# Kernel optimization log

Hardware: AMD Instinct MI355X
Metric: run time of the kernel (lower is better)

The kernel has to match this reference:

```python
import jax, jax.numpy as jnp
import numpy as np

DIM = 2048
N_HEADS = 16
N_KV_HEADS = 4
HEAD_DIM = DIM // N_HEADS  # 128
ROPE_BASE = 10000.0
QK_GAIN_INIT = 1.0
RMS_EPS = 1.1920928955078125e-07  # torch F.rms_norm default eps = finfo(fp32).eps


def _rms_norm(x):
    # normalize over last dim, no learned gain
    var = jnp.mean(jnp.square(x), axis=-1, keepdims=True)
    return x * jax.lax.rsqrt(var + RMS_EPS)


def _rope_cos_sin(seq_len, dtype):
    half = HEAD_DIM // 2
    inv_freq = 1.0 / (ROPE_BASE ** (jnp.arange(0, HEAD_DIM, 2, dtype=jnp.float32) / HEAD_DIM))
    t = jnp.arange(seq_len, dtype=jnp.float32)
    freqs = jnp.outer(t, inv_freq)  # [S, half]
    return jnp.cos(freqs).astype(dtype), jnp.sin(freqs).astype(dtype)


def _apply_rotary(x, cos, sin):
    # x: [B, H, S, D]; cos/sin: [S, D//2] broadcast over B,H
    half = x.shape[-1] // 2
    x1, x2 = x[..., :half], x[..., half:]
    return jnp.concatenate((x1 * cos + x2 * sin, x1 * (-sin) + x2 * cos), axis=-1)


def setup_inputs() -> dict:
    key = jax.random.key(0)
    ks = jax.random.split(key, 6)
    B, S = 2, 2048
    kv_dim = N_KV_HEADS * HEAD_DIM
    x = jax.random.normal(ks[0], (B, S, DIM), dtype=jnp.float32)
    Wq = jax.random.normal(ks[1], (DIM, DIM), dtype=jnp.float32) * (DIM ** -0.5)
    Wk = jax.random.normal(ks[2], (kv_dim, DIM), dtype=jnp.float32) * (DIM ** -0.5)
    Wv = jax.random.normal(ks[3], (kv_dim, DIM), dtype=jnp.float32) * (DIM ** -0.5)
    Wproj = jax.random.normal(ks[4], (DIM, DIM), dtype=jnp.float32) * (DIM ** -0.5)
    q_gain = jnp.full((N_HEADS,), QK_GAIN_INIT, dtype=jnp.float32)
    return {"x": x, "Wq": Wq, "Wk": Wk, "Wv": Wv, "Wproj": Wproj, "q_gain": q_gain}


def reference(x, Wq, Wk, Wv, Wproj, q_gain):
    B, S, D = x.shape
    G = N_HEADS // N_KV_HEADS  # GQA group size
    # QKV projections (CastedLinear, no bias)
    q = (x @ Wq.T).reshape(B, S, N_HEADS, HEAD_DIM).transpose(0, 2, 1, 3)      # [B,H,S,d]
    k = (x @ Wk.T).reshape(B, S, N_KV_HEADS, HEAD_DIM).transpose(0, 2, 1, 3)   # [B,Hkv,S,d]
    v = (x @ Wv.T).reshape(B, S, N_KV_HEADS, HEAD_DIM).transpose(0, 2, 1, 3)
    # QK RMS-norm
    q = _rms_norm(q)
    k = _rms_norm(k)
    # RoPE (scaling='none' -> attention_factor = 1.0)
    cos, sin = _rope_cos_sin(S, q.dtype)
    q = _apply_rotary(q, cos, sin)
    k = _apply_rotary(k, cos, sin)
    # per-head query gain * attention_factor (=1.0)
    q = q * q_gain.astype(q.dtype)[None, :, None, None]
    # causal GQA SDPA: group queries by kv head, no k/v materialized repeats
    qg = q.reshape(B, N_KV_HEADS, G, S, HEAD_DIM)
    scale = 1.0 / jnp.sqrt(jnp.asarray(HEAD_DIM, dtype=q.dtype))
    scores = jnp.einsum('bkgqd,bkld->bkgql', qg, k) * scale  # [B,Hkv,G,S,S]
    causal = jnp.tril(jnp.ones((S, S), dtype=bool))
    scores = jnp.where(causal, scores, jnp.asarray(-jnp.inf, dtype=scores.dtype))
    attn = jax.nn.softmax(scores, axis=-1)
    y = jnp.einsum('bkgql,bkld->bkgqd', attn, v)              # [B,Hkv,G,S,d]
    y = y.reshape(B, N_HEADS, S, HEAD_DIM).transpose(0, 2, 1, 3).reshape(B, S, D)
    return y @ Wproj.T
```

## Files before the change

kernel.cpp:

```cpp
#include <hip/hip_runtime.h>
#include <hip/hip_bf16.h>

#define DIM 2048
#define NH 16
#define NKV 4
#define HD 128
#define S_LEN 2048
#define BATCH 2
#define QKV_N 3072
#define NEGBIG -1.0e30f

typedef __attribute__((ext_vector_type(8))) short bf16x8;
typedef __attribute__((ext_vector_type(4))) float f32x4;
typedef unsigned short ushort_t;

#define GLOAD_LDS16(gp, lp)                                                       \
    __builtin_amdgcn_global_load_lds(                                             \
        (const __attribute__((address_space(1))) void*)(gp),                      \
        (__attribute__((address_space(3))) void*)(lp), 16, 0, 0)

static __device__ __forceinline__ ushort_t f2bf(float f) {
    union { float f; unsigned u; } v; v.f = f;
    unsigned r = v.u + 0x7fffu + ((v.u >> 16) & 1u);
    return (ushort_t)(r >> 16);
}
static __device__ __forceinline__ float bf2f(ushort_t u) {
    union { unsigned u; float f; } v; v.u = ((unsigned)u) << 16;
    return v.f;
}
static __device__ __forceinline__ unsigned pk2bf(float a, float b) {
    unsigned r;
    __asm__ volatile("v_cvt_pk_bf16_f32 %0, %1, %2" : "=v"(r) : "v"(a), "v"(b));
    return r;
}

__global__ __launch_bounds__(256) void cvt_bf16(const float* __restrict__ src,
                                                ushort_t* __restrict__ dst, int n) {
    int i = (blockIdx.x * 256 + threadIdx.x) * 4;
    if (i >= n) return;
    float4 v = *(const float4*)&src[i];
    uint2 o = {pk2bf(v.x, v.y), pk2bf(v.z, v.w)};
    *(uint2*)&dst[i] = o;
}

__global__ __launch_bounds__(256) void cvt_w3(const float* __restrict__ Wq,
                                              const float* __restrict__ Wk,
                                              const float* __restrict__ Wv,
                                              ushort_t* __restrict__ dst) {
    int i = (blockIdx.x * 256 + threadIdx.x) * 4;
    const float* src;
    int off;
    if (i < 4194304) { src = Wq; off = i; }
    else if (i < 5242880) { src = Wk; off = i - 4194304; }
    else { src = Wv; off = i - 5242880; }
    float4 v = *(const float4*)&src[off];
    uint2 o = {pk2bf(v.x, v.y), pk2bf(v.z, v.w)};
    *(uint2*)&dst[i] = o;
}

static __device__ __forceinline__ void store_c(float* p, float v) { *p = v; }
static __device__ __forceinline__ void store_c(ushort_t* p, float v) { *p = f2bf(v); }

template <typename OutT>
__global__ __launch_bounds__(256) void gemm_bt(const ushort_t* __restrict__ A,
                                               const ushort_t* __restrict__ B,
                                               OutT* __restrict__ C,
                                               int M, int N, int K) {
    __shared__ __align__(16) ushort_t As[2][128 * 32];
    __shared__ __align__(16) ushort_t Bs[2][128 * 32];
    const int t = threadIdx.x;
    const int lane = t & 63;
    const int wave = t >> 6;
    const int m16 = lane & 15;
    const int quad = lane >> 4;
    const int wr = wave >> 1;
    const int wc = wave & 1;
    const int m0 = blockIdx.y * 128;
    const int n0 = blockIdx.x * 128;

    f32x4 acc[4][4];
#pragma unroll
    for (int i = 0; i < 4; i++)
#pragma unroll
        for (int j = 0; j < 4; j++) acc[i][j] = (f32x4){0.f, 0.f, 0.f, 0.f};

    const int r0 = t >> 2;
    const int c8 = (t & 3) * 8;

#pragma unroll
    for (int half = 0; half < 2; ++half) {
        GLOAD_LDS16(&A[(size_t)(m0 + half * 64 + r0) * K + c8],
                    &As[0][(half * 64 + wave * 16) * 32]);
        GLOAD_LDS16(&B[(size_t)(n0 + half * 64 + r0) * K + c8],
                    &Bs[0][(half * 64 + wave * 16) * 32]);
    }
    for (int k0 = 0; k0 < K; k0 += 32) {
        const int cur = (k0 >> 5) & 1;
        __syncthreads();
        if (k0 + 32 < K) {
#pragma unroll
            for (int half = 0; half < 2; ++half) {
                GLOAD_LDS16(&A[(size_t)(m0 + half * 64 + r0) * K + k0 + 32 + c8],
                            &As[cur ^ 1][(half * 64 + wave * 16) * 32]);
                GLOAD_LDS16(&B[(size_t)(n0 + half * 64 + r0) * K + k0 + 32 + c8],
                            &Bs[cur ^ 1][(half * 64 + wave * 16) * 32]);
            }
        }
        bf16x8 af[4], bfr[4];
#pragma unroll
        for (int mt = 0; mt < 4; mt++)
            af[mt] = *(const bf16x8*)&As[cur][(wr * 64 + mt * 16 + m16) * 32 + quad * 8];
#pragma unroll
        for (int nt = 0; nt < 4; nt++)
            bfr[nt] = *(const bf16x8*)&Bs[cur][(wc * 64 + nt * 16 + m16) * 32 + quad * 8];
#pragma unroll
        for (int mt = 0; mt < 4; mt++)
#pragma unroll
            for (int nt = 0; nt < 4; nt++)
                acc[mt][nt] = __builtin_amdgcn_mfma_f32_16x16x32_bf16(af[mt], bfr[nt],
                                                                      acc[mt][nt], 0, 0, 0);
    }
#pragma unroll
    for (int mt = 0; mt < 4; mt++) {
#pragma unroll
        for (int r = 0; r < 4; r++) {
            int row = m0 + wr * 64 + mt * 16 + quad * 4 + r;
#pragma unroll
            for (int nt = 0; nt < 4; nt++) {
                int col = n0 + wc * 64 + nt * 16 + m16;
                store_c(&C[(size_t)row * N + col], acc[mt][nt][r]);
            }
        }
    }
}

__global__ __launch_bounds__(256) void rope_qk(ushort_t* __restrict__ qkv,
                                               const float* __restrict__ gain) {
    const int wave = threadIdx.x >> 6, lane = threadIdx.x & 63;
    int r = blockIdx.x * 4 + wave;
    ushort_t* p;
    float g;
    int s;
    if (r < 65536) {
        const int h = r & (NH - 1);
        const int bs = r >> 4;
        s = bs & (S_LEN - 1);
        p = qkv + (size_t)bs * QKV_N + h * HD;
        g = gain[h];
    } else {
        r -= 65536;
        const int kv = r & (NKV - 1);
        const int bs = r >> 2;
        s = bs & (S_LEN - 1);
        p = qkv + (size_t)bs * QKV_N + DIM + kv * HD;
        g = 1.0f;
    }
    float x1 = bf2f(p[lane]);
    float x2 = bf2f(p[lane + 64]);
    float ss = x1 * x1 + x2 * x2;
#pragma unroll
    for (int m = 32; m >= 1; m >>= 1) ss += __shfl_xor(ss, m, 64);
    float rms = rsqrtf(ss * (1.0f / 128.0f) + 1.1920928955078125e-07f);
    x1 *= rms; x2 *= rms;
    float invf = powf(10000.0f, -(float)lane * (1.0f / 64.0f));
    float fr = (float)s * invf;
    float c = cosf(fr), sn = sinf(fr);
    p[lane] = f2bf((x1 * c + x2 * sn) * g);
    p[lane + 64] = f2bf((x2 * c - x1 * sn) * g);
}

__global__ __launch_bounds__(256) void vtrans(const ushort_t* __restrict__ qkv,
                                              ushort_t* __restrict__ vt) {
    __shared__ ushort_t tile[64][72];
    const int s0 = blockIdx.x * 64, d0 = blockIdx.y * 64;
    const int kv = blockIdx.z & (NKV - 1), b = blockIdx.z >> 2;
    const int t = threadIdx.x;
    const int r = t >> 2, cg = (t & 3) * 16;
    const ushort_t* src = qkv + ((size_t)(b * S_LEN + s0 + r)) * QKV_N + (DIM + NKV * HD) +
                          kv * HD + d0 + cg;
    *(uint4*)&tile[r][cg] = *(const uint4*)&src[0];
    *(uint4*)&tile[r][cg + 8] = *(const uint4*)&src[8];
    __syncthreads();
    ushort_t ov[16];
#pragma unroll
    for (int j = 0; j < 16; j++) ov[j] = tile[cg + j][r];
    ushort_t* dst = vt + ((size_t)((b * NKV + kv) * HD + d0 + r)) * S_LEN + s0 + cg;
    *(uint4*)&dst[0] = *(uint4*)&ov[0];
    *(uint4*)&dst[8] = *(uint4*)&ov[8];
}

__device__ __constant__ short attn_tab[24][4] = {
    {15, 0, 16, 14}, {15, 16, 32, 15}, {7, 0, 16, -1}, {14, 0, 15, 12},
    {13, 0, 14, 10}, {13, 14, 28, 11}, {6, 0, 14, -1}, {10, 0, 11, 4},
    {12, 0, 13, 8},  {12, 13, 26, 9}, {14, 15, 30, 13}, {11, 0, 12, 6},
    {11, 12, 24, 7}, {5, 0, 12, -1}, {10, 11, 22, 5},  {9, 0, 10, 2},
    {2, 0, 6, -1},   {1, 0, 4, -1},  {0, 0, 2, -1},    {3, 0, 8, -1},
    {8, 0, 9, 0},    {8, 9, 18, 1},  {9, 10, 20, 3},   {4, 0, 10, -1},
};

__global__ __launch_bounds__(256) void attn(const ushort_t* __restrict__ QKV,
                                            const ushort_t* __restrict__ Vt,
                                            ushort_t* __restrict__ Y,
                                            ushort_t* __restrict__ Po,
                                            float* __restrict__ Pl) {
    __shared__ __align__(16) ushort_t Ks[64 * 128];
    __shared__ __align__(16) ushort_t Vs[128 * 64];
    __shared__ __align__(16) ushort_t Ps[4][32 * 72];
    const int lane = threadIdx.x & 63;
    const int wave = threadIdx.x >> 6;
    const int m16 = lane & 15, quad = lane >> 4;
    const int seg = blockIdx.x >> 5;
    const int hb = blockIdx.x & 31;
    const int h = hb & (NH - 1), b = hb >> 4;
    const int kvh = h >> 2;
    const int bx = attn_tab[seg][0];
    const int t0 = attn_tab[seg][1];
    const int t1 = attn_tab[seg][2];
    const int slotl = attn_tab[seg][3];
    const int q0w = bx * 128 + wave * 32;

    const ushort_t* kbase = QKV + (size_t)b * S_LEN * QKV_N + DIM + kvh * HD;
    const ushort_t* vbase = Vt + (size_t)(b * NKV + kvh) * (HD * S_LEN);

    bf16x8 bq[2][4];
#pragma unroll
    for (int g = 0; g < 2; g++)
#pragma unroll
        for (int ks = 0; ks < 4; ks++)
            bq[g][ks] = *(const bf16x8*)&QKV[((size_t)(b * S_LEN + q0w + g * 16 + m16)) * QKV_N +
                                             h * HD + ks * 32 + quad * 8];

    float ls[2] = {0.f, 0.f};
    f32x4 o[2][8];
#pragma unroll
    for (int g = 0; g < 2; g++)
#pragma unroll
        for (int nd = 0; nd < 8; nd++) o[g][nd] = (f32x4){0.f, 0.f, 0.f, 0.f};

    ushort_t* pw = Ps[wave];
    for (int t = t0; t < t1; ++t) {
        const int kv0 = t * 64;
        __syncthreads();
#pragma unroll
        for (int i = 0; i < 4; i++) {
            const int c0 = i * 256 + wave * 64;
            const int ck = c0 + lane;
            const int krow = ck >> 4;
            const int kcol = (ck & 15) ^ (krow & 7);
            GLOAD_LDS16(kbase + (size_t)(kv0 + krow) * QKV_N + kcol * 8, &Ks[c0 * 8]);
            const int vd = ck >> 3;
            const int vcol = (ck & 7) ^ (vd & 7);
            GLOAD_LDS16(vbase + (size_t)vd * S_LEN + kv0 + vcol * 8, &Vs[c0 * 8]);
        }
        __syncthreads();

        f32x4 st[2][4];
#pragma unroll
        for (int g = 0; g < 2; g++)
#pragma unroll
            for (int nt = 0; nt < 4; nt++) st[g][nt] = (f32x4){0.f, 0.f, 0.f, 0.f};
#pragma unroll
        for (int ks = 0; ks < 4; ks++)
#pragma unroll
            for (int nt = 0; nt < 4; nt++) {
                const int row = nt * 16 + m16;
                bf16x8 ak = *(const bf16x8*)&Ks[row * 128 + (((ks * 4 + quad) ^ (row & 7)) * 8)];
#pragma unroll
                for (int g = 0; g < 2; g++)
                    st[g][nt] = __builtin_amdgcn_mfma_f32_16x16x32_bf16(ak, bq[g][ks],
                                                                        st[g][nt], 0, 0, 0);
            }
#pragma unroll
        for (int g = 0; g < 2; g++) {
            const int q0g = q0w + g * 16;
            const int qg = q0g + m16;
            const bool interior = (kv0 + 63 <= q0g);
            float rs = 0.f;
#pragma unroll
            for (int nt = 0; nt < 4; nt++) {
                float p[4];
#pragma unroll
                for (int r = 0; r < 4; r++) {
                    float x = st[g][nt][r] * 0.08838834764831845f;
                    if (!interior) {
                        const int kg = kv0 + nt * 16 + quad * 4 + r;
                        x = (kg > qg) ? NEGBIG : x;
                    }
                    p[r] = __expf(x);
                }
                rs += (p[0] + p[1]) + (p[2] + p[3]);
                uint2 pk = {pk2bf(p[0], p[1]), pk2bf(p[2], p[3])};
                *(uint2*)&pw[(g * 16 + m16) * 72 + nt * 16 + quad * 4] = pk;
            }
            ls[g] += rs;
        }
        __asm__ __volatile__("s_waitcnt lgkmcnt(0)" ::: "memory");
        bf16x8 bp[2][2];
#pragma unroll
        for (int g = 0; g < 2; g++)
#pragma unroll
            for (int kk = 0; kk < 2; kk++)
                bp[g][kk] = *(const bf16x8*)&pw[(g * 16 + m16) * 72 + kk * 32 + quad * 8];
#pragma unroll
        for (int kk = 0; kk < 2; kk++)
#pragma unroll
            for (int nd = 0; nd < 8; nd++) {
                const int vrow = nd * 16 + m16;
                bf16x8 av = *(const bf16x8*)&Vs[vrow * 64 + (((kk * 4 + quad) ^ (vrow & 7)) * 8)];
#pragma unroll
                for (int g = 0; g < 2; g++)
                    o[g][nd] = __builtin_amdgcn_mfma_f32_16x16x32_bf16(av, bp[g][kk],
                                                                       o[g][nd], 0, 0, 0);
            }
    }
    float l_tot[2];
#pragma unroll
    for (int g = 0; g < 2; g++) {
        float v = ls[g];
        v += __shfl_xor(v, 16, 64);
        v += __shfl_xor(v, 32, 64);
        l_tot[g] = v;
    }
    if (slotl < 0) {
#pragma unroll
        for (int g = 0; g < 2; g++) {
            const float inv = 1.0f / l_tot[g];
            const int qg = q0w + g * 16 + m16;
            ushort_t* yp = Y + ((size_t)(b * S_LEN + qg)) * DIM + h * HD;
#pragma unroll
            for (int nd = 0; nd < 8; nd++) {
                uint2 pk = {pk2bf(o[g][nd][0] * inv, o[g][nd][1] * inv),
                            pk2bf(o[g][nd][2] * inv, o[g][nd][3] * inv)};
                *(uint2*)&yp[nd * 16 + quad * 4] = pk;
            }
        }
    } else {
        const int slot = ((b * NH + h) << 4) + slotl;
        ushort_t* po = Po + (size_t)slot * (128 * 128);
#pragma unroll
        for (int g = 0; g < 2; g++) {
            const int ql = wave * 32 + g * 16 + m16;
#pragma unroll
            for (int nd = 0; nd < 8; nd++) {
                uint2 pk = {pk2bf(o[g][nd][0], o[g][nd][1]),
                            pk2bf(o[g][nd][2], o[g][nd][3])};
                *(uint2*)&po[ql * 128 + nd * 16 + quad * 4] = pk;
            }
            if (quad == 0) Pl[slot * 128 + ql] = l_tot[g];
        }
    }
}

__global__ __launch_bounds__(256) void attn_combine(const ushort_t* __restrict__ Po,
                                                    const float* __restrict__ Pl,
                                                    ushort_t* __restrict__ Y) {
    const int R = blockIdx.x * 2 + (threadIdx.x >> 7);
    const int d = threadIdx.x & 127;
    const int q = R & 127;
    const int bx8 = (R >> 7) & 7;
    const int h = (R >> 10) & 15;
    const int b = R >> 14;
    const int slot0 = ((b * NH + h) << 4) + bx8 * 2;
    const float l0 = Pl[slot0 * 128 + q], l1 = Pl[(slot0 + 1) * 128 + q];
    const float inv = 1.0f / (l0 + l1);
    const float o0 = bf2f(Po[(size_t)slot0 * (128 * 128) + q * 128 + d]);
    const float o1 = bf2f(Po[(size_t)(slot0 + 1) * (128 * 128) + q * 128 + d]);
    const int qg = (bx8 + 8) * 128 + q;
    Y[((size_t)(b * S_LEN + qg)) * DIM + h * HD + d] = f2bf((o0 + o1) * inv);
}

extern "C" void kernel_launch(void* const* d_in, const int* in_sizes, int n_in,
                              void* d_out, int out_size, void* d_ws, size_t ws_size,
                              hipStream_t stream) {
    (void)in_sizes; (void)n_in; (void)out_size; (void)ws_size;
    const float* xf  = (const float*)d_in[0];
    const float* Wqf = (const float*)d_in[1];
    const float* Wkf = (const float*)d_in[2];
    const float* Wvf = (const float*)d_in[3];
    const float* Wpf = (const float*)d_in[4];
    const float* gn  = (const float*)d_in[5];
    float* out = (float*)d_out;

    char* ws = (char*)d_ws;
    ushort_t* xb    = (ushort_t*)(ws);
    ushort_t* qkv   = (ushort_t*)(ws + (16ull << 20));
    ushort_t* vt    = (ushort_t*)(ws + (40ull << 20));
    ushort_t* Wqkvb = (ushort_t*)(ws + (44ull << 20));
    ushort_t* Wpb   = (ushort_t*)(ws + (56ull << 20));
    ushort_t* y     = xb;
    ushort_t* Po    = (ushort_t*)(ws + (44ull << 20));
    float*    Pl    = (float*)(ws + (60ull << 20));

    const int M = BATCH * S_LEN;
    cvt_bf16<<<dim3(M * DIM / 1024), 256, 0, stream>>>(xf, xb, M * DIM);
    cvt_w3<<<dim3(QKV_N * DIM / 1024), 256, 0, stream>>>(Wqf, Wkf, Wvf, Wqkvb);
    gemm_bt<<<dim3(QKV_N / 128, M / 128), 256, 0, stream>>>(xb, Wqkvb, qkv, M, QKV_N, DIM);
    rope_qk<<<dim3(M * (NH + NKV) / 4), 256, 0, stream>>>(qkv, gn);
    vtrans<<<dim3(S_LEN / 64, HD / 64, BATCH * NKV), 256, 0, stream>>>(qkv, vt);
    attn<<<dim3(768, 1, 1), 256, 0, stream>>>(qkv, vt, y, Po, Pl);
    attn_combine<<<dim3(BATCH * NH * 8 * 128 / 2), 256, 0, stream>>>(Po, Pl, y);
    cvt_bf16<<<dim3(DIM * DIM / 1024), 256, 0, stream>>>(Wpf, Wpb, DIM * DIM);
    gemm_bt<<<dim3(DIM / 128, M / 128), 256, 0, stream>>>(y, Wpb, out, M, DIM, DIM);
}
```

Baseline: 333.5 us.

## Fuse input conversions, fuse RoPE/norm and V transpose into QKV GEMM epilogue

```diff
diff --git a/kernel.cpp b/kernel.cpp
--- a/kernel.cpp
+++ b/kernel.cpp
@@ -34,28 +34,33 @@
     return r;
 }
 
-__global__ __launch_bounds__(256) void cvt_bf16(const float* __restrict__ src,
-                                                ushort_t* __restrict__ dst, int n) {
-    int i = (blockIdx.x * 256 + threadIdx.x) * 4;
-    if (i >= n) return;
-    float4 v = *(const float4*)&src[i];
-    uint2 o = {pk2bf(v.x, v.y), pk2bf(v.z, v.w)};
-    *(uint2*)&dst[i] = o;
-}
-
-__global__ __launch_bounds__(256) void cvt_w3(const float* __restrict__ Wq,
+__global__ __launch_bounds__(256) void cvt_in(const float* __restrict__ x,
+                                              const float* __restrict__ Wq,
                                               const float* __restrict__ Wk,
                                               const float* __restrict__ Wv,
-                                              ushort_t* __restrict__ dst) {
+                                              const float* __restrict__ Wp,
+                                              ushort_t* __restrict__ xb,
+                                              ushort_t* __restrict__ Wqkvb,
+                                              ushort_t* __restrict__ Wpb) {
     int i = (blockIdx.x * 256 + threadIdx.x) * 4;
     const float* src;
-    int off;
-    if (i < 4194304) { src = Wq; off = i; }
-    else if (i < 5242880) { src = Wk; off = i - 4194304; }
-    else { src = Wv; off = i - 5242880; }
-    float4 v = *(const float4*)&src[off];
+    ushort_t* dst;
+    int soff, doff;
+    if (i < 8388608) {
+        src = x; dst = xb; soff = i; doff = i;
+    } else if (i < 14680064) {
+        int j = i - 8388608;
+        dst = Wqkvb; doff = j;
+        if (j < 4194304) { src = Wq; soff = j; }
+        else if (j < 5242880) { src = Wk; soff = j - 4194304; }
+        else { src = Wv; soff = j - 5242880; }
+    } else {
+        int j = i - 14680064;
+        src = Wp; dst = Wpb; soff = j; doff = j;
+    }
+    float4 v = *(const float4*)&src[soff];
     uint2 o = {pk2bf(v.x, v.y), pk2bf(v.z, v.w)};
-    *(uint2*)&dst[i] = o;
+    *(uint2*)&dst[doff] = o;
 }
 
 static __device__ __forceinline__ void store_c(float* p, float v) { *p = v; }
@@ -66,8 +71,8 @@
                                                const ushort_t* __restrict__ B,
                                                OutT* __restrict__ C,
                                                int M, int N, int K) {
-    __shared__ __align__(16) ushort_t As[2][128 * 32];
-    __shared__ __align__(16) ushort_t Bs[2][128 * 32];
+    __shared__ __align__(16) ushort_t As[128 * 64];
+    __shared__ __align__(16) ushort_t Bs[128 * 64];
     const int t = threadIdx.x;
     const int lane = t & 63;
     const int wave = t >> 6;
@@ -84,41 +89,40 @@
 #pragma unroll
         for (int j = 0; j < 4; j++) acc[i][j] = (f32x4){0.f, 0.f, 0.f, 0.f};
 
-    const int r0 = t >> 2;
-    const int c8 = (t & 3) * 8;
-
-#pragma unroll
-    for (int half = 0; half < 2; ++half) {
-        GLOAD_LDS16(&A[(size_t)(m0 + half * 64 + r0) * K + c8],
-                    &As[0][(half * 64 + wave * 16) * 32]);
-        GLOAD_LDS16(&B[(size_t)(n0 + half * 64 + r0) * K + c8],
-                    &Bs[0][(half * 64 + wave * 16) * 32]);
-    }
-    for (int k0 = 0; k0 < K; k0 += 32) {
-        const int cur = (k0 >> 5) & 1;
-        __syncthreads();
-        if (k0 + 32 < K) {
-#pragma unroll
-            for (int half = 0; half < 2; ++half) {
-                GLOAD_LDS16(&A[(size_t)(m0 + half * 64 + r0) * K + k0 + 32 + c8],
-                            &As[cur ^ 1][(half * 64 + wave * 16) * 32]);
-                GLOAD_LDS16(&B[(size_t)(n0 + half * 64 + r0) * K + k0 + 32 + c8],
-                            &Bs[cur ^ 1][(half * 64 + wave * 16) * 32]);
-            }
-        }
-        bf16x8 af[4], bfr[4];
-#pragma unroll
-        for (int mt = 0; mt < 4; mt++)
-            af[mt] = *(const bf16x8*)&As[cur][(wr * 64 + mt * 16 + m16) * 32 + quad * 8];
-#pragma unroll
-        for (int nt = 0; nt < 4; nt++)
-            bfr[nt] = *(const bf16x8*)&Bs[cur][(wc * 64 + nt * 16 + m16) * 32 + quad * 8];
-#pragma unroll
-        for (int mt = 0; mt < 4; mt++)
-#pragma unroll
-            for (int nt = 0; nt < 4; nt++)
-                acc[mt][nt] = __builtin_amdgcn_mfma_f32_16x16x32_bf16(af[mt], bfr[nt],
-                                                                      acc[mt][nt], 0, 0, 0);
+    const int rsub = lane >> 3;
+    const int csw0 = lane & 7;
+
+    for (int k0 = 0; k0 < K; k0 += 64) {
+#pragma unroll
+        for (int i = 0; i < 4; ++i) {
+            const int rowb = wave * 32 + i * 8;
+            const int row = rowb + rsub;
+            const int gc = (csw0 ^ (row & 7)) * 8;
+            GLOAD_LDS16(&A[(size_t)(m0 + row) * K + k0 + gc], &As[rowb * 64]);
+            GLOAD_LDS16(&B[(size_t)(n0 + row) * K + k0 + gc], &Bs[rowb * 64]);
+        }
+        __syncthreads();
+#pragma unroll
+        for (int ks = 0; ks < 2; ks++) {
+            bf16x8 af[4], bfr[4];
+#pragma unroll
+            for (int mt = 0; mt < 4; mt++) {
+                const int row = wr * 64 + mt * 16 + m16;
+                af[mt] = *(const bf16x8*)&As[row * 64 + (((ks * 4 + quad) ^ (row & 7)) * 8)];
+            }
+#pragma unroll
+            for (int nt = 0; nt < 4; nt++) {
+                const int row = wc * 64 + nt * 16 + m16;
+                bfr[nt] = *(const bf16x8*)&Bs[row * 64 + (((ks * 4 + quad) ^ (row & 7)) * 8)];
+            }
+#pragma unroll
+            for (int mt = 0; mt < 4; mt++)
+#pragma unroll
+                for (int nt = 0; nt < 4; nt++)
+                    acc[mt][nt] = __builtin_amdgcn_mfma_f32_16x16x32_bf16(af[mt], bfr[nt],
+                                                                          acc[mt][nt], 0, 0, 0);
+        }
+        __syncthreads();
     }
 #pragma unroll
     for (int mt = 0; mt < 4; mt++) {
@@ -134,59 +138,115 @@
     }
 }
 
-__global__ __launch_bounds__(256) void rope_qk(ushort_t* __restrict__ qkv,
-                                               const float* __restrict__ gain) {
-    const int wave = threadIdx.x >> 6, lane = threadIdx.x & 63;
-    int r = blockIdx.x * 4 + wave;
-    ushort_t* p;
-    float g;
-    int s;
-    if (r < 65536) {
-        const int h = r & (NH - 1);
-        const int bs = r >> 4;
-        s = bs & (S_LEN - 1);
-        p = qkv + (size_t)bs * QKV_N + h * HD;
-        g = gain[h];
+__global__ __launch_bounds__(256) void gemm_qkv(const ushort_t* __restrict__ A,
+                                                const ushort_t* __restrict__ B,
+                                                ushort_t* __restrict__ qkv,
+                                                ushort_t* __restrict__ vt,
+                                                const float* __restrict__ gain) {
+    __shared__ __align__(16) ushort_t sh[2][128 * 64];
+    ushort_t* As = sh[0];
+    ushort_t* Bs = sh[1];
+    ushort_t* Cs = &sh[0][0];
+    const int t = threadIdx.x;
+    const int lane = t & 63;
+    const int wave = t >> 6;
+    const int m16 = lane & 15;
+    const int quad = lane >> 4;
+    const int wr = wave >> 1;
+    const int wc = wave & 1;
+    const int m0 = blockIdx.y * 128;
+    const int bx = blockIdx.x;
+    const int n0 = bx * 128;
+    const int K = DIM;
+
+    f32x4 acc[4][4];
+#pragma unroll
+    for (int i = 0; i < 4; i++)
+#pragma unroll
+        for (int j = 0; j < 4; j++) acc[i][j] = (f32x4){0.f, 0.f, 0.f, 0.f};
+
+    const int rsub = lane >> 3;
+    const int csw0 = lane & 7;
+
+    for (int k0 = 0; k0 < K; k0 += 64) {
+#pragma unroll
+        for (int i = 0; i < 4; ++i) {
+            const int rowb = wave * 32 + i * 8;
+            const int row = rowb + rsub;
+            const int gc = (csw0 ^ (row & 7)) * 8;
+            GLOAD_LDS16(&A[(size_t)(m0 + row) * K + k0 + gc], &As[rowb * 64]);
+            GLOAD_LDS16(&B[(size_t)(n0 + row) * K + k0 + gc], &Bs[rowb * 64]);
+        }
+        __syncthreads();
+#pragma unroll
+        for (int ks = 0; ks < 2; ks++) {
+            bf16x8 af[4], bfr[4];
+#pragma unroll
+            for (int mt = 0; mt < 4; mt++) {
+                const int row = wr * 64 + mt * 16 + m16;
+                af[mt] = *(const bf16x8*)&As[row * 64 + (((ks * 4 + quad) ^ (row & 7)) * 8)];
+            }
+#pragma unroll
+            for (int nt = 0; nt < 4; nt++) {
+                const int row = wc * 64 + nt * 16 + m16;
+                bfr[nt] = *(const bf16x8*)&Bs[row * 64 + (((ks * 4 + quad) ^ (row & 7)) * 8)];
+            }
+#pragma unroll
+            for (int mt = 0; mt < 4; mt++)
+#pragma unroll
+                for (int nt = 0; nt < 4; nt++)
+                    acc[mt][nt] = __builtin_amdgcn_mfma_f32_16x16x32_bf16(af[mt], bfr[nt],
+                                                                          acc[mt][nt], 0, 0, 0);
+        }
+        __syncthreads();
+    }
+#pragma unroll
+    for (int mt = 0; mt < 4; mt++)
+#pragma unroll
+        for (int r = 0; r < 4; r++) {
+            const int row = wr * 64 + mt * 16 + quad * 4 + r;
+#pragma unroll
+            for (int nt = 0; nt < 4; nt++)
+                Cs[row * 128 + wc * 64 + nt * 16 + m16] = f2bf(acc[mt][nt][r]);
+        }
+    __syncthreads();
+
+    if (bx < 20) {
+        const float g = (bx < 16) ? gain[bx] : 1.0f;
+        const float invf = exp2f(-0.20762050593046f * (float)lane);
+#pragma unroll 4
+        for (int i = 0; i < 32; i++) {
+            const int row = wave * 32 + i;
+            const int m = m0 + row;
+            const int s = m & (S_LEN - 1);
+            float x1 = bf2f(Cs[row * 128 + lane]);
+            float x2 = bf2f(Cs[row * 128 + lane + 64]);
+            float ss = x1 * x1 + x2 * x2;
+#pragma unroll
+            for (int mm = 32; mm >= 1; mm >>= 1) ss += __shfl_xor(ss, mm, 64);
+            const float rms = rsqrtf(ss * (1.0f / 128.0f) + 1.1920928955078125e-07f);
+            x1 *= rms; x2 *= rms;
+            const float fr = (float)s * invf;
+            const float c = cosf(fr), sn = sinf(fr);
+            ushort_t* dst = qkv + (size_t)m * QKV_N + bx * 128;
+            dst[lane] = f2bf((x1 * c + x2 * sn) * g);
+            dst[lane + 64] = f2bf((x2 * c - x1 * sn) * g);
+        }
     } else {
-        r -= 65536;
-        const int kv = r & (NKV - 1);
-        const int bs = r >> 2;
-        s = bs & (S_LEN - 1);
-        p = qkv + (size_t)bs * QKV_N + DIM + kv * HD;
-        g = 1.0f;
-    }
-    float x1 = bf2f(p[lane]);
-    float x2 = bf2f(p[lane + 64]);
-    float ss = x1 * x1 + x2 * x2;
-#pragma unroll
-    for (int m = 32; m >= 1; m >>= 1) ss += __shfl_xor(ss, m, 64);
-    float rms = rsqrtf(ss * (1.0f / 128.0f) + 1.1920928955078125e-07f);
-    x1 *= rms; x2 *= rms;
-    float invf = powf(10000.0f, -(float)lane * (1.0f / 64.0f));
-    float fr = (float)s * invf;
-    float c = cosf(fr), sn = sinf(fr);
-    p[lane] = f2bf((x1 * c + x2 * sn) * g);
-    p[lane + 64] = f2bf((x2 * c - x1 * sn) * g);
-}
-
-__global__ __launch_bounds__(256) void vtrans(const ushort_t* __restrict__ qkv,
-                                              ushort_t* __restrict__ vt) {
-    __shared__ ushort_t tile[64][72];
-    const int s0 = blockIdx.x * 64, d0 = blockIdx.y * 64;
-    const int kv = blockIdx.z & (NKV - 1), b = blockIdx.z >> 2;
-    const int t = threadIdx.x;
-    const int r = t >> 2, cg = (t & 3) * 16;
-    const ushort_t* src = qkv + ((size_t)(b * S_LEN + s0 + r)) * QKV_N + (DIM + NKV * HD) +
-                          kv * HD + d0 + cg;
-    *(uint4*)&tile[r][cg] = *(const uint4*)&src[0];
-    *(uint4*)&tile[r][cg + 8] = *(const uint4*)&src[8];
-    __syncthreads();
-    ushort_t ov[16];
-#pragma unroll
-    for (int j = 0; j < 16; j++) ov[j] = tile[cg + j][r];
-    ushort_t* dst = vt + ((size_t)((b * NKV + kv) * HD + d0 + r)) * S_LEN + s0 + cg;
-    *(uint4*)&dst[0] = *(uint4*)&ov[0];
-    *(uint4*)&dst[8] = *(uint4*)&ov[8];
+        const int d = t >> 1;
+        const int so = (t & 1) * 64;
+        const int b = m0 >> 11;
+        const int s0 = m0 & (S_LEN - 1);
+        const int kv = bx - 20;
+        ushort_t* dst = vt + ((size_t)(b * NKV + kv) * HD + d) * S_LEN + s0 + so;
+#pragma unroll
+        for (int j0 = 0; j0 < 64; j0 += 8) {
+            ushort_t tmp[8];
+#pragma unroll
+            for (int j = 0; j < 8; j++) tmp[j] = Cs[(so + j0 + j) * 128 + d];
+            *(uint4*)&dst[j0] = *(uint4*)tmp;
+        }
+    }
 }
 
 __device__ __constant__ short attn_tab[24][4] = {
@@ -334,9 +394,23 @@
                 *(uint2*)&yp[nd * 16 + quad * 4] = pk;
             }
         }
+    } else if ((slotl & 1) == 0) {
+        const int slot = ((b * NH + h) << 4) + slotl;
+#pragma unroll
+        for (int g = 0; g < 2; g++) {
+            const int qg = q0w + g * 16 + m16;
+            ushort_t* yp = Y + ((size_t)(b * S_LEN + qg)) * DIM + h * HD;
+#pragma unroll
+            for (int nd = 0; nd < 8; nd++) {
+                uint2 pk = {pk2bf(o[g][nd][0], o[g][nd][1]),
+                            pk2bf(o[g][nd][2], o[g][nd][3])};
+                *(uint2*)&yp[nd * 16 + quad * 4] = pk;
+            }
+            if (quad == 0) Pl[slot * 128 + wave * 32 + g * 16 + m16] = l_tot[g];
+        }
     } else {
         const int slot = ((b * NH + h) << 4) + slotl;
-        ushort_t* po = Po + (size_t)slot * (128 * 128);
+        ushort_t* po = Po + (size_t)(((b * NH + h) << 3) + (slotl >> 1)) * (128 * 128);
 #pragma unroll
         for (int g = 0; g < 2; g++) {
             const int ql = wave * 32 + g * 16 + m16;
@@ -360,13 +434,15 @@
     const int bx8 = (R >> 7) & 7;
     const int h = (R >> 10) & 15;
     const int b = R >> 14;
-    const int slot0 = ((b * NH + h) << 4) + bx8 * 2;
-    const float l0 = Pl[slot0 * 128 + q], l1 = Pl[(slot0 + 1) * 128 + q];
+    const int hb16 = ((b * NH + h) << 4);
+    const float l0 = Pl[(hb16 + bx8 * 2) * 128 + q];
+    const float l1 = Pl[(hb16 + bx8 * 2 + 1) * 128 + q];
     const float inv = 1.0f / (l0 + l1);
-    const float o0 = bf2f(Po[(size_t)slot0 * (128 * 128) + q * 128 + d]);
-    const float o1 = bf2f(Po[(size_t)(slot0 + 1) * (128 * 128) + q * 128 + d]);
     const int qg = (bx8 + 8) * 128 + q;
-    Y[((size_t)(b * S_LEN + qg)) * DIM + h * HD + d] = f2bf((o0 + o1) * inv);
+    ushort_t* yp = Y + ((size_t)(b * S_LEN + qg)) * DIM + h * HD + d;
+    const float o0 = bf2f(*yp);
+    const float o1 = bf2f(Po[(size_t)(((b * NH + h) << 3) + bx8) * (128 * 128) + q * 128 + d]);
+    *yp = f2bf((o0 + o1) * inv);
 }
 
 extern "C" void kernel_launch(void* const* d_in, const int* in_sizes, int n_in,
@@ -389,16 +465,12 @@
     ushort_t* Wpb   = (ushort_t*)(ws + (56ull << 20));
     ushort_t* y     = xb;
     ushort_t* Po    = (ushort_t*)(ws + (44ull << 20));
-    float*    Pl    = (float*)(ws + (60ull << 20));
+    float*    Pl    = (float*)(ws + (52ull << 20));
 
     const int M = BATCH * S_LEN;
-    cvt_bf16<<<dim3(M * DIM / 1024), 256, 0, stream>>>(xf, xb, M * DIM);
-    cvt_w3<<<dim3(QKV_N * DIM / 1024), 256, 0, stream>>>(Wqf, Wkf, Wvf, Wqkvb);
-    gemm_bt<<<dim3(QKV_N / 128, M / 128), 256, 0, stream>>>(xb, Wqkvb, qkv, M, QKV_N, DIM);
-    rope_qk<<<dim3(M * (NH + NKV) / 4), 256, 0, stream>>>(qkv, gn);
-    vtrans<<<dim3(S_LEN / 64, HD / 64, BATCH * NKV), 256, 0, stream>>>(qkv, vt);
+    cvt_in<<<dim3(18432), 256, 0, stream>>>(xf, Wqf, Wkf, Wvf, Wpf, xb, Wqkvb, Wpb);
+    gemm_qkv<<<dim3(QKV_N / 128, M / 128), 256, 0, stream>>>(xb, Wqkvb, qkv, vt, gn);
     attn<<<dim3(768, 1, 1), 256, 0, stream>>>(qkv, vt, y, Po, Pl);
     attn_combine<<<dim3(BATCH * NH * 8 * 128 / 2), 256, 0, stream>>>(Po, Pl, y);
-    cvt_bf16<<<dim3(DIM * DIM / 1024), 256, 0, stream>>>(Wpf, Wpb, DIM * DIM);
     gemm_bt<<<dim3(DIM / 128, M / 128), 256, 0, stream>>>(y, Wpb, out, M, DIM, DIM);
 }
```

New measurement: 305.0 us. 1.09x faster.
